# Optimization experiments

Hardware: AMD Instinct MI355X
Metric: run time of the kernel (lower is better)

Reference implementation:

```python
import jax, jax.numpy as jnp
import numpy as np

EPS = 1e-5  # torch GroupNorm default
KNN_K = 16


def _knn_idx(Q, P, K):
    # Q:[B,Nq,3], P:[B,Np,3] -> idx [B,Nq,K], ascending squared distance
    d = (jnp.sum(Q * Q, -1)[:, :, None] + jnp.sum(P * P, -1)[:, None, :]
         - 2.0 * jnp.einsum('bqc,bkc->bqk', Q, P))
    _, idx = jax.lax.top_k(-d, K)
    return idx


def _gather_nbr(feat_bnc, idx_bqk):
    # feat:[B,Np,C], idx:[B,Nq,K] -> [B,Nq,K,C]  (knn_gather)
    return jax.vmap(lambda f, i: f[i])(feat_bnc, idx_bqk)


def _group_norm(x_bcnk, gamma, beta, num_groups=8):
    B, C, N, K = x_bcnk.shape
    G = min(num_groups, C)
    xg = x_bcnk.reshape(B, G, C // G, N, K)
    mu = xg.mean(axis=(2, 3, 4), keepdims=True)
    var = xg.var(axis=(2, 3, 4), keepdims=True)
    xn = ((xg - mu) / jnp.sqrt(var + EPS)).reshape(B, C, N, K)
    return xn * gamma[None, :, None, None] + beta[None, :, None, None]


def _edge_conv(Fq_bcn, Fk_bcn, Pq_b3n, Pk_b3n, k, W, gamma, beta):
    # EdgeConv: concat(x_j - x_i, x_i) -> conv1x1 -> GN -> ReLU -> max over K
    idx = _knn_idx(Pq_b3n.transpose(0, 2, 1), Pk_b3n.transpose(0, 2, 1), k)
    nbr = _gather_nbr(Fk_bcn.transpose(0, 2, 1), idx)          # [B,Nq,K,Cin]
    Fi = jnp.broadcast_to(Fq_bcn.transpose(0, 2, 1)[:, :, None, :], nbr.shape)
    pair = jnp.concatenate([nbr - Fi, Fi], axis=-1)            # [B,Nq,K,2Cin]
    out = jnp.einsum('oc,bnkc->bonk', W, pair)                 # conv 1x1, no bias
    out = _group_norm(out, gamma, beta)
    out = jax.nn.relu(out)
    return out.max(axis=-1)                                    # [B,Cout,Nq]


def _fps_idx(P_b3n, m):
    # Farthest point sampling starting at index 0 (pytorch3d default)
    def one(Pn3):
        d0 = jnp.sum((Pn3 - Pn3[0]) ** 2, -1)
        def step(dists, _):
            nxt = jnp.argmax(dists)
            d = jnp.sum((Pn3 - Pn3[nxt]) ** 2, -1)
            return jnp.minimum(dists, d), nxt
        _, idxs = jax.lax.scan(step, d0, None, length=m - 1)
        return jnp.concatenate([jnp.zeros((1,), jnp.int32), idxs.astype(jnp.int32)])
    return jax.vmap(one)(P_b3n.transpose(0, 2, 1))


def _gather_bcn(x_bcn, idx_bm):
    return jax.vmap(lambda x, i: x[:, i])(x_bcn, idx_bm)


def setup_inputs() -> dict:
    key = jax.random.key(0)
    ks = jax.random.split(key, 8)
    B, N = 2, 8192
    def w(k, shape, s=0.1):
        return jax.random.normal(k, shape, jnp.float32) * s
    return {
        'xyz': jax.random.normal(ks[0], (B, 3, N), jnp.float32),
        'stem_w': w(ks[1], (8, 3)), 'stem_b': jnp.zeros((8,), jnp.float32),
        'w1': w(ks[2], (32, 16)),  'g1': jnp.ones((32,), jnp.float32),  'b1': jnp.zeros((32,), jnp.float32),
        'w2': w(ks[3], (64, 64)),  'g2': jnp.ones((64,), jnp.float32),  'b2': jnp.zeros((64,), jnp.float32),
        'w3': w(ks[4], (64, 128)), 'g3': jnp.ones((64,), jnp.float32),  'b3': jnp.zeros((64,), jnp.float32),
        'w4': w(ks[5], (128, 128)),'g4': jnp.ones((128,), jnp.float32), 'b4': jnp.zeros((128,), jnp.float32),
    }


def reference(xyz, stem_w, stem_b, w1, g1, b1, w2, g2, b2, w3, g3, b3, w4, g4, b4):
    K = KNN_K
    P0 = xyz                                                     # [B,3,N0]
    F0 = jnp.einsum('oc,bcn->bon', stem_w, xyz) + stem_b[None, :, None]
    F0a = _edge_conv(F0, F0, P0, P0, K, w1, g1, b1)              # [B,32,N0]
    N0 = P0.shape[2]
    N1 = max(1, N0 // 4)
    idx1 = _fps_idx(P0, N1)
    P1 = _gather_bcn(P0, idx1)
    F1sk = _gather_bcn(F0a, idx1)
    F1a = _edge_conv(F1sk, F0a, P1, P0, K, w2, g2, b2)           # [B,64,N1]
    N2 = max(1, N1 // 4)
    idx2 = _fps_idx(P1, N2)
    P2 = _gather_bcn(P1, idx2)
    F2sk = _gather_bcn(F1a, idx2)
    F2mid = _edge_conv(F2sk, F1a, P2, P1, K, w3, g3, b3)         # [B,64,N2]
    F2a = _edge_conv(F2mid, F1a, P2, P1, K, w4, g4, b4)          # [B,128,N2]
    return (P0, F0a, P1, F1a, P2, F2a)
```

## Files before the change

kernel.cpp:

```cpp
#include <hip/hip_runtime.h>
#include <math.h>

typedef unsigned long long ull;

__global__ __launch_bounds__(256) void stem_fused(const float* __restrict__ xyz,
    const float* __restrict__ w, const float* __restrict__ bias,
    float* __restrict__ F0, float* __restrict__ P0o, int N){
  int id = blockIdx.x*256 + threadIdx.x;
  int n = id % N; int b = id / N;
  float x = xyz[((size_t)b*3+0)*N+n];
  float y = xyz[((size_t)b*3+1)*N+n];
  float z = xyz[((size_t)b*3+2)*N+n];
  P0o[((size_t)b*3+0)*N+n] = x;
  P0o[((size_t)b*3+1)*N+n] = y;
  P0o[((size_t)b*3+2)*N+n] = z;
  #pragma unroll
  for (int o=0;o<8;o++){
    float v = fmaf(w[o*3+0],x, fmaf(w[o*3+1],y, fmaf(w[o*3+2],z, bias[o])));
    F0[((size_t)b*8+o)*N+n] = v;
  }
}

__global__ __launch_bounds__(256) void knn_fused(
    const float* __restrict__ Pq, const float* __restrict__ Pp,
    int* __restrict__ idxk, int Nq, int Np){
  __shared__ float4 tile[4][256];
  __shared__ float  pd[16][4][64];
  __shared__ int    pi[16][4][64];
  int t = threadIdx.x, w = t>>6, l = t&63;
  int b = blockIdx.y;
  int qn = blockIdx.x*64 + l;
  const float* Pqb = Pq + (size_t)b*3*Nq;
  const float* Ppb = Pp + (size_t)b*3*Np;
  float qx = Pqb[qn], qy = Pqb[Nq+qn], qz = Pqb[2*Nq+qn];
  float qq = __fadd_rn(__fadd_rn(__fmul_rn(qx,qx),__fmul_rn(qy,qy)),__fmul_rn(qz,qz));

  float dl[16]; int il[16];
  #pragma unroll
  for (int u=0;u<16;u++){ dl[u]=INFINITY; il[u]=-1; }
  float maxd = INFINITY; int maxslot = 0;

  int CANDS = Np >> 2;
  int c0 = w*CANDS;
  for (int tb=0; tb<CANDS; tb+=256){
    __syncthreads();
    #pragma unroll
    for (int k=0;k<4;k++){
      int p = c0 + tb + k*64 + l;
      float px = Ppb[p], py = Ppb[Np+p], pz = Ppb[2*Np+p];
      float pp = __fadd_rn(__fadd_rn(__fmul_rn(px,px),__fmul_rn(py,py)),__fmul_rn(pz,pz));
      tile[w][k*64+l] = make_float4(px,py,pz,pp);
    }
    __syncthreads();
    for (int j=0;j<256;j++){
      float4 c = tile[w][j];
      float dot = __fadd_rn(__fadd_rn(__fmul_rn(qx,c.x),__fmul_rn(qy,c.y)),__fmul_rn(qz,c.z));
      float dc  = __fsub_rn(__fadd_rn(qq,c.w), __fmul_rn(2.0f,dot));
      if (dc < maxd){
        int pidx = c0 + tb + j;
        #pragma unroll
        for (int u=0;u<16;u++){ bool sel=(maxslot==u); dl[u]=sel?dc:dl[u]; il[u]=sel?pidx:il[u]; }
        maxd = dl[0]; maxslot = 0;
        #pragma unroll
        for (int u=1;u<16;u++){ bool g=(dl[u]>maxd); maxd=g?dl[u]:maxd; maxslot=g?u:maxslot; }
      }
    }
  }
  #pragma unroll
  for (int u=0;u<16;u++){ pd[u][w][l]=dl[u]; pi[u][w][l]=il[u]; }
  __syncthreads();
  if (t < 64){
    int q = t;
    float mdl[16]; int mil[16];
    #pragma unroll
    for (int u=0;u<16;u++){ mdl[u]=INFINITY; mil[u]=0x7fffffff; }
    float mmaxd = INFINITY; int mmaxi = 0x7fffffff; int mslot = 0;
    for (int s=0;s<4;s++){
      #pragma unroll
      for (int u=0;u<16;u++){
        float d = pd[u][s][q]; int ii = pi[u][s][q];
        bool better = (d < mmaxd) || (d == mmaxd && ii < mmaxi);
        if (better){
          #pragma unroll
          for (int v=0;v<16;v++){ bool sel=(mslot==v); mdl[v]=sel?d:mdl[v]; mil[v]=sel?ii:mil[v]; }
          mmaxd = mdl[0]; mmaxi = mil[0]; mslot = 0;
          #pragma unroll
          for (int v=1;v<16;v++){
            bool g = (mdl[v]>mmaxd) || (mdl[v]==mmaxd && mil[v]>mmaxi);
            mmaxd=g?mdl[v]:mmaxd; mmaxi=g?mil[v]:mmaxi; mslot=g?v:mslot;
          }
        }
      }
    }
    #pragma unroll
    for (int u=0;u<16;u++)
      idxk[((size_t)b*Nq + blockIdx.x*64 + q)*16 + u] = mil[u];
  }
}

template<int CIN, int COUT>
__global__ __launch_bounds__(1024) void edge_conv_pre(
    const float* __restrict__ Fk, const float* __restrict__ Fi,
    const int* __restrict__ idx, const float* __restrict__ W,
    float* __restrict__ pre, int Nq, int Np){
  constexpr int C2  = 2*CIN;
  constexpr int PAD = C2 + 4;
  constexpr int TO  = (COUT <= 64) ? COUT : 64;
  constexpr int OP  = COUT / TO;
  extern __shared__ float sm[];
  float* Wl = sm;
  float* Pl = sm + COUT*PAD;
  int t = threadIdx.x;
  int n = blockIdx.x, b = blockIdx.y;
  for (int e=t; e<COUT*C2; e += blockDim.x){
    int o=e/C2, c=e%C2; Wl[o*PAD+c] = W[e];
  }
  const int* idxn = idx + ((size_t)b*Nq + n)*16;
  for (int e=t; e<16*C2; e += blockDim.x){
    int k = e/C2, c = e%C2;
    int cc = (c < CIN) ? c : (c-CIN);
    float fi = Fi[((size_t)b*CIN + cc)*Nq + n];
    float v;
    if (c < CIN){ int nb = idxn[k]; v = Fk[((size_t)b*CIN + c)*Np + nb] - fi; }
    else v = fi;
    Pl[k*PAD+c] = v;
  }
  __syncthreads();
  int k = t & 15, o0 = t >> 4;
  #pragma unroll
  for (int op=0; op<OP; op++){
    int o = o0 + op*TO;
    float acc = 0.f;
    #pragma unroll
    for (int c=0;c<C2;c+=4){
      float4 wv = *(const float4*)&Wl[o*PAD+c];
      float4 pv = *(const float4*)&Pl[k*PAD+c];
      acc = fmaf(wv.x,pv.x,acc); acc = fmaf(wv.y,pv.y,acc);
      acc = fmaf(wv.z,pv.z,acc); acc = fmaf(wv.w,pv.w,acc);
    }
    pre[(((size_t)b*COUT + o)*Nq + n)*16 + k] = acc;
  }
}

template<int COUT>
__global__ __launch_bounds__(1024) void gn_fused(const float* __restrict__ pre,
    const float* __restrict__ gamma, const float* __restrict__ beta,
    float* __restrict__ outF, int Nq){
  constexpr int CPG = COUT/8;
  int g = blockIdx.x, b = blockIdx.y, t = threadIdx.x;
  size_t base = (((size_t)b*COUT + g*CPG)*(size_t)Nq)*16;
  const float* p = pre + base;
  int len = CPG*Nq*16;
  double s=0.0, sq=0.0;
  for (int i = t*4; i < len; i += 4096){
    float4 v = *(const float4*)(p+i);
    s += (double)v.x; sq = fma((double)v.x,(double)v.x,sq);
    s += (double)v.y; sq = fma((double)v.y,(double)v.y,sq);
    s += (double)v.z; sq = fma((double)v.z,(double)v.z,sq);
    s += (double)v.w; sq = fma((double)v.w,(double)v.w,sq);
  }
  #pragma unroll
  for (int off=32; off>=1; off>>=1){ s += __shfl_down(s, off); sq += __shfl_down(sq, off); }
  __shared__ double ls[16], lq[16];
  __shared__ float stats[2];
  int wid = t>>6;
  if ((t&63)==0){ ls[wid]=s; lq[wid]=sq; }
  __syncthreads();
  if (t==0){
    double S=0.0, Q=0.0;
    #pragma unroll
    for (int w=0;w<16;w++){ S+=ls[w]; Q+=lq[w]; }
    double cnt = (double)CPG*(double)Nq*16.0;
    double mu  = S/cnt;
    double var = Q/cnt - mu*mu;
    stats[0] = (float)mu;
    stats[1] = (float)(1.0/sqrt(var+1e-5));
  }
  __syncthreads();
  float muf = stats[0], rstd = stats[1];
  int outs = CPG*Nq;
  for (int e=t; e<outs; e+=1024){
    int ol = e/Nq, n = e - ol*Nq;
    int o = g*CPG + ol;
    float ga = gamma[o], be = beta[o];
    const float4* pp = (const float4*)(p + (size_t)e*16);
    float m = 0.f;
    #pragma unroll
    for (int q=0;q<4;q++){
      float4 v = pp[q];
      m = fmaxf(m, fmaf((v.x-muf)*rstd, ga, be));
      m = fmaxf(m, fmaf((v.y-muf)*rstd, ga, be));
      m = fmaxf(m, fmaf((v.z-muf)*rstd, ga, be));
      m = fmaxf(m, fmaf((v.w-muf)*rstd, ga, be));
    }
    outF[((size_t)b*COUT + o)*Nq + n] = m;
  }
}

template<int CTRL>
__device__ __forceinline__ float dpp_maxf(float x){
  int y = __builtin_amdgcn_update_dpp(0, __float_as_int(x), CTRL, 0xf, 0xf, true);
  return fmaxf(x, __int_as_float(y));
}

template<int PPT, int BLK, int M>
__global__ __launch_bounds__(BLK, 1) void fps_kernel(const float* __restrict__ P,
    int* __restrict__ idx_out){
  constexpr int N  = PPT*BLK;
  constexpr int NW = BLK/64;
  extern __shared__ __align__(16) float sm[];
  float* lx = sm; float* ly = sm+N; float* lz = sm+2*N;
  ull* wk = (ull*)(sm + 3*N);
  int b = blockIdx.x, t = threadIdx.x;
  const float* Pb = P + (size_t)b*3*N;
  for (int i=t; i<N; i+=BLK){ lx[i]=Pb[i]; ly[i]=Pb[N+i]; lz[i]=Pb[2*N+i]; }
  __syncthreads();
  float px[PPT], py[PPT], pz[PPT], dist[PPT];
  #pragma unroll
  for (int j=0;j<PPT;j++){ int p=t*PPT+j; px[j]=lx[p]; py[j]=ly[p]; pz[j]=lz[p]; }
  #pragma unroll
  for (int j=0;j<PPT;j++){
    asm volatile("" : "+v"(px[j]), "+v"(py[j]), "+v"(pz[j]));
  }
  float sx = lx[0], sy = ly[0], sz = lz[0];
  float bd = -1.f; int bj = 0;
  #pragma unroll
  for (int j=0;j<PPT;j++){
    float dx=__fsub_rn(px[j],sx), dy=__fsub_rn(py[j],sy), dz=__fsub_rn(pz[j],sz);
    float dd=__fadd_rn(__fadd_rn(__fmul_rn(dx,dx),__fmul_rn(dy,dy)),__fmul_rn(dz,dz));
    dist[j]=dd;
    bool c = dd > bd; bd = c?dd:bd; bj = c?j:bj;
  }
  int pbest = t*PPT + bj;
  if (t==0) idx_out[(size_t)b*M] = 0;
  int wid = t>>6, lane = t&63, par = 0;
  for (int i=1;i<M;i++){
    float r = bd;
    r = dpp_maxf<0x111>(r); r = dpp_maxf<0x112>(r);
    r = dpp_maxf<0x114>(r); r = dpp_maxf<0x118>(r);
    r = dpp_maxf<0x142>(r); r = dpp_maxf<0x143>(r);
    float wmax = __int_as_float(__builtin_amdgcn_readlane(__float_as_int(r), 63));
    ull msk = __ballot(bd == wmax);
    int srcl = __ffsll(msk) - 1;
    int wp = __builtin_amdgcn_readlane(pbest, srcl);
    if (lane==0)
      wk[par*NW + wid] = ((ull)__float_as_uint(wmax)<<32)
                       | (unsigned)(~(unsigned)wp);
    __syncthreads();
    ull best = wk[par*NW];
    #pragma unroll
    for (int w=1;w<NW;w++){ ull o = wk[par*NW+w]; best = (o>best)?o:best; }
    unsigned widx = ~(unsigned)best;
    if (t==0) idx_out[(size_t)b*M + i] = (int)widx;
    float nsx = lx[widx], nsy = ly[widx], nsz = lz[widx];
    par ^= 1;
    float nbd = -1.f; int nbj = 0;
    #pragma unroll
    for (int j=0;j<PPT;j++){
      float dx=__fsub_rn(px[j],nsx), dy=__fsub_rn(py[j],nsy), dz=__fsub_rn(pz[j],nsz);
      float dd=__fadd_rn(__fadd_rn(__fmul_rn(dx,dx),__fmul_rn(dy,dy)),__fmul_rn(dz,dz));
      float nd = fminf(dist[j], dd);
      dist[j] = nd;
      bool c = nd > nbd; nbd = c?nd:nbd; nbj = c?j:nbj;
    }
    bd = nbd; pbest = t*PPT + nbj;
  }
}

__global__ __launch_bounds__(256) void gather_fused(float* __restrict__ Pdst,
    const float* __restrict__ Psrc, float* __restrict__ Fdst,
    const float* __restrict__ Fsrc, const int* __restrict__ idxv,
    int CF, int Nsrc, int M){
  int per = (3+CF)*M;
  int total = 2*per;
  for (int id = blockIdx.x*256 + threadIdx.x; id < total; id += gridDim.x*256){
    int b = id/per, r = id%per, c = r/M, m = r%M;
    int sn = idxv[(size_t)b*M + m];
    if (c < 3)
      Pdst[((size_t)b*3+c)*M+m] = Psrc[((size_t)b*3+c)*Nsrc+sn];
    else {
      int cf = c-3;
      Fdst[((size_t)b*CF+cf)*M+m] = Fsrc[((size_t)b*CF+cf)*Nsrc+sn];
    }
  }
}

extern "C" void kernel_launch(void* const* d_in, const int* in_sizes, int n_in,
                              void* d_out, int out_size, void* d_ws, size_t ws_size,
                              hipStream_t stream) {
  const float* xyz    = (const float*)d_in[0];
  const float* stem_w = (const float*)d_in[1];
  const float* stem_b = (const float*)d_in[2];
  const float* w1 = (const float*)d_in[3];
  const float* g1 = (const float*)d_in[4];
  const float* b1 = (const float*)d_in[5];
  const float* w2 = (const float*)d_in[6];
  const float* g2 = (const float*)d_in[7];
  const float* b2 = (const float*)d_in[8];
  const float* w3 = (const float*)d_in[9];
  const float* g3 = (const float*)d_in[10];
  const float* b3 = (const float*)d_in[11];
  const float* w4 = (const float*)d_in[12];
  const float* g4 = (const float*)d_in[13];
  const float* b4 = (const float*)d_in[14];

  float* out = (float*)d_out;
  float* P0o  = out + 0;
  float* F0a  = out + 49152;
  float* P1o  = out + 573440;
  float* F1a  = out + 585728;
  float* P2o  = out + 847872;
  float* F2a  = out + 850944;

  char* ws = (char*)d_ws;
  float* F0     = (float*)(ws + 0);
  float* pre    = (float*)(ws + 524288);
  int*   idxk   = (int*)  (ws + 34078720);
  int*   idx1   = (int*)  (ws + 35127296);
  int*   idx2   = (int*)  (ws + 35143680);
  float* F1sk   = (float*)(ws + 35147776);
  float* F2sk   = (float*)(ws + 35672064);
  float* F2mid  = (float*)(ws + 35934208);

  size_t smem_c1 = (size_t)(32*20  + 16*20 )*4;
  size_t smem_c2 = (size_t)(64*68  + 16*68 )*4;
  size_t smem_c3 = (size_t)(64*132 + 16*132)*4;
  size_t smem_c4 = (size_t)(128*132+ 16*132)*4;
  size_t smem_f1 = (size_t)3*8192*4 + 256;
  size_t smem_f2 = (size_t)3*2048*4 + 256;

  stem_fused<<<64, 256, 0, stream>>>(xyz, stem_w, stem_b, F0, P0o, 8192);
  knn_fused<<<dim3(128,2), 256, 0, stream>>>(xyz, xyz, idxk, 8192, 8192);
  edge_conv_pre<8,32><<<dim3(8192,2), 512, smem_c1, stream>>>(F0, F0, idxk, w1, pre, 8192, 8192);
  gn_fused<32><<<dim3(8,2), 1024, 0, stream>>>(pre, g1, b1, F0a, 8192);

  fps_kernel<32,256,2048><<<2, 256, smem_f1, stream>>>(xyz, idx1);
  gather_fused<<<560, 256, 0, stream>>>(P1o, xyz, F1sk, F0a, idx1, 32, 8192, 2048);

  knn_fused<<<dim3(32,2), 256, 0, stream>>>(P1o, xyz, idxk, 2048, 8192);
  edge_conv_pre<32,64><<<dim3(2048,2), 1024, smem_c2, stream>>>(F0a, F1sk, idxk, w2, pre, 2048, 8192);
  gn_fused<64><<<dim3(8,2), 1024, 0, stream>>>(pre, g2, b2, F1a, 2048);

  fps_kernel<8,256,512><<<2, 256, smem_f2, stream>>>(P1o, idx2);
  gather_fused<<<268, 256, 0, stream>>>(P2o, P1o, F2sk, F1a, idx2, 64, 2048, 512);

  knn_fused<<<dim3(8,2), 256, 0, stream>>>(P2o, P1o, idxk, 512, 2048);
  edge_conv_pre<64,64><<<dim3(512,2), 1024, smem_c3, stream>>>(F1a, F2sk, idxk, w3, pre, 512, 2048);
  gn_fused<64><<<dim3(8,2), 1024, 0, stream>>>(pre, g3, b3, F2mid, 512);

  edge_conv_pre<64,128><<<dim3(512,2), 1024, smem_c4, stream>>>(F1a, F2mid, idxk, w4, pre, 512, 2048);
  gn_fused<128><<<dim3(8,2), 1024, 0, stream>>>(pre, g4, b4, F2a, 512);

  (void)in_sizes; (void)n_in; (void)out_size; (void)ws_size;
}
```

Before: 3.484 ms.

## Fuse GroupNorm partial stats into edge conv and split FPS argmax chains

Each edge-conv block now reduces sum and sum-of-squares for its outputs with wave shuffles and writes per-group partials. A small combine kernel turns these into mean and rstd, and a fully parallel apply kernel does normalize, ReLU and max-over-K. This replaces the old 16-block GroupNorm kernel, which reread the whole pre-activation buffer twice with too few blocks. FPS also splits its per-thread argmax into four independent chains to shorten the dependency chain in the serial loop, at the cost of float partial sums and workspace aliasing of the partial buffers.

```diff
diff --git a/kernel.cpp b/kernel.cpp
--- a/kernel.cpp
+++ b/kernel.cpp
@@ -102,11 +102,14 @@
 __global__ __launch_bounds__(1024) void edge_conv_pre(
     const float* __restrict__ Fk, const float* __restrict__ Fi,
     const int* __restrict__ idx, const float* __restrict__ W,
-    float* __restrict__ pre, int Nq, int Np){
+    float* __restrict__ pre, float* __restrict__ partS,
+    float* __restrict__ partQ, int pstride, int Nq, int Np){
   constexpr int C2  = 2*CIN;
   constexpr int PAD = C2 + 4;
   constexpr int TO  = (COUT <= 64) ? COUT : 64;
   constexpr int OP  = COUT / TO;
+  constexpr int CPG = COUT/8;
+  constexpr int WPG = CPG/4;
   extern __shared__ float sm[];
   float* Wl = sm;
   float* Pl = sm + COUT*PAD;
@@ -127,6 +130,7 @@
   }
   __syncthreads();
   int k = t & 15, o0 = t >> 4;
+  float accv[OP];
   #pragma unroll
   for (int op=0; op<OP; op++){
     int o = o0 + op*TO;
@@ -138,63 +142,68 @@
       acc = fmaf(wv.x,pv.x,acc); acc = fmaf(wv.y,pv.y,acc);
       acc = fmaf(wv.z,pv.z,acc); acc = fmaf(wv.w,pv.w,acc);
     }
+    accv[op] = acc;
     pre[(((size_t)b*COUT + o)*Nq + n)*16 + k] = acc;
   }
-}
-
-template<int COUT>
-__global__ __launch_bounds__(1024) void gn_fused(const float* __restrict__ pre,
-    const float* __restrict__ gamma, const float* __restrict__ beta,
-    float* __restrict__ outF, int Nq){
-  constexpr int CPG = COUT/8;
-  int g = blockIdx.x, b = blockIdx.y, t = threadIdx.x;
-  size_t base = (((size_t)b*COUT + g*CPG)*(size_t)Nq)*16;
-  const float* p = pre + base;
-  int len = CPG*Nq*16;
-  double s=0.0, sq=0.0;
-  for (int i = t*4; i < len; i += 4096){
-    float4 v = *(const float4*)(p+i);
-    s += (double)v.x; sq = fma((double)v.x,(double)v.x,sq);
-    s += (double)v.y; sq = fma((double)v.y,(double)v.y,sq);
-    s += (double)v.z; sq = fma((double)v.z,(double)v.z,sq);
-    s += (double)v.w; sq = fma((double)v.w,(double)v.w,sq);
-  }
-  #pragma unroll
-  for (int off=32; off>=1; off>>=1){ s += __shfl_down(s, off); sq += __shfl_down(sq, off); }
-  __shared__ double ls[16], lq[16];
-  __shared__ float stats[2];
+  int w = t>>6;
+  #pragma unroll
+  for (int op=0; op<OP; op++){
+    float s1 = accv[op], s2 = accv[op]*accv[op];
+    #pragma unroll
+    for (int off=32; off>=1; off>>=1){ s1 += __shfl_down(s1,off); s2 += __shfl_down(s2,off); }
+    if ((t&63)==0){
+      int o = o0 + op*TO;
+      int g = o / CPG;
+      int slot = n*WPG + (w % WPG);
+      partS[((size_t)(b*8+g))*pstride + slot] = s1;
+      partQ[((size_t)(b*8+g))*pstride + slot] = s2;
+    }
+  }
+}
+
+__global__ __launch_bounds__(256) void gn_combine(const float* __restrict__ partS,
+    const float* __restrict__ partQ, float2* __restrict__ stats,
+    int nslot, int pstride, double cnt){
+  int bg = blockIdx.x, t = threadIdx.x;
+  const float* ps = partS + (size_t)bg*pstride;
+  const float* pq = partQ + (size_t)bg*pstride;
+  double s=0.0, q=0.0;
+  for (int i=t; i<nslot; i+=256){ s += (double)ps[i]; q += (double)pq[i]; }
+  #pragma unroll
+  for (int off=32; off>=1; off>>=1){ s += __shfl_down(s,off); q += __shfl_down(q,off); }
+  __shared__ double ls[4], lq[4];
   int wid = t>>6;
-  if ((t&63)==0){ ls[wid]=s; lq[wid]=sq; }
+  if ((t&63)==0){ ls[wid]=s; lq[wid]=q; }
   __syncthreads();
   if (t==0){
-    double S=0.0, Q=0.0;
-    #pragma unroll
-    for (int w=0;w<16;w++){ S+=ls[w]; Q+=lq[w]; }
-    double cnt = (double)CPG*(double)Nq*16.0;
-    double mu  = S/cnt;
+    double S=ls[0]+ls[1]+ls[2]+ls[3], Q=lq[0]+lq[1]+lq[2]+lq[3];
+    double mu = S/cnt;
     double var = Q/cnt - mu*mu;
-    stats[0] = (float)mu;
-    stats[1] = (float)(1.0/sqrt(var+1e-5));
-  }
-  __syncthreads();
-  float muf = stats[0], rstd = stats[1];
-  int outs = CPG*Nq;
-  for (int e=t; e<outs; e+=1024){
-    int ol = e/Nq, n = e - ol*Nq;
-    int o = g*CPG + ol;
-    float ga = gamma[o], be = beta[o];
-    const float4* pp = (const float4*)(p + (size_t)e*16);
-    float m = 0.f;
-    #pragma unroll
-    for (int q=0;q<4;q++){
-      float4 v = pp[q];
-      m = fmaxf(m, fmaf((v.x-muf)*rstd, ga, be));
-      m = fmaxf(m, fmaf((v.y-muf)*rstd, ga, be));
-      m = fmaxf(m, fmaf((v.z-muf)*rstd, ga, be));
-      m = fmaxf(m, fmaf((v.w-muf)*rstd, ga, be));
-    }
-    outF[((size_t)b*COUT + o)*Nq + n] = m;
-  }
+    stats[bg] = make_float2((float)mu, (float)(1.0/sqrt(var+1e-5)));
+  }
+}
+
+template<int COUT>
+__global__ __launch_bounds__(256) void gn_apply(const float* __restrict__ pre,
+    const float2* __restrict__ stats, const float* __restrict__ gamma,
+    const float* __restrict__ beta, float* __restrict__ outF, int Nq){
+  int id = blockIdx.x*256 + threadIdx.x;
+  int o = (id/Nq)%COUT; int b = id/(Nq*COUT);
+  int g = o/(COUT/8);
+  float2 st = stats[b*8+g];
+  float muf = st.x, rstd = st.y;
+  float ga=gamma[o], be=beta[o];
+  const float4* p = (const float4*)(pre + (size_t)id*16);
+  float m = 0.f;
+  #pragma unroll
+  for (int q=0;q<4;q++){
+    float4 v = p[q];
+    m = fmaxf(m, fmaf((v.x-muf)*rstd, ga, be));
+    m = fmaxf(m, fmaf((v.y-muf)*rstd, ga, be));
+    m = fmaxf(m, fmaf((v.z-muf)*rstd, ga, be));
+    m = fmaxf(m, fmaf((v.w-muf)*rstd, ga, be));
+  }
+  outF[id] = m;
 }
 
 template<int CTRL>
@@ -208,6 +217,7 @@
     int* __restrict__ idx_out){
   constexpr int N  = PPT*BLK;
   constexpr int NW = BLK/64;
+  constexpr int Q  = PPT/4;
   extern __shared__ __align__(16) float sm[];
   float* lx = sm; float* ly = sm+N; float* lz = sm+2*N;
   ull* wk = (ull*)(sm + 3*N);
@@ -254,16 +264,23 @@
     if (t==0) idx_out[(size_t)b*M + i] = (int)widx;
     float nsx = lx[widx], nsy = ly[widx], nsz = lz[widx];
     par ^= 1;
-    float nbd = -1.f; int nbj = 0;
+    float nb0=-1.f, nb1=-1.f, nb2=-1.f, nb3=-1.f;
+    int   nj0=0,    nj1=0,    nj2=0,    nj3=0;
     #pragma unroll
     for (int j=0;j<PPT;j++){
       float dx=__fsub_rn(px[j],nsx), dy=__fsub_rn(py[j],nsy), dz=__fsub_rn(pz[j],nsz);
       float dd=__fadd_rn(__fadd_rn(__fmul_rn(dx,dx),__fmul_rn(dy,dy)),__fmul_rn(dz,dz));
       float nd = fminf(dist[j], dd);
       dist[j] = nd;
-      bool c = nd > nbd; nbd = c?nd:nbd; nbj = c?j:nbj;
-    }
-    bd = nbd; pbest = t*PPT + nbj;
+      if (j < Q)        { bool c = nd > nb0; nb0 = c?nd:nb0; nj0 = c?j:nj0; }
+      else if (j < 2*Q) { bool c = nd > nb1; nb1 = c?nd:nb1; nj1 = c?j:nj1; }
+      else if (j < 3*Q) { bool c = nd > nb2; nb2 = c?nd:nb2; nj2 = c?j:nj2; }
+      else              { bool c = nd > nb3; nb3 = c?nd:nb3; nj3 = c?j:nj3; }
+    }
+    bool ca = nb1 > nb0; float ta = ca?nb1:nb0; int tja = ca?nj1:nj0;
+    bool cb = nb3 > nb2; float tb = cb?nb3:nb2; int tjb = cb?nj3:nj2;
+    bool cc = tb > ta;   bd = cc?tb:ta;         int nbj = cc?tjb:tja;
+    pbest = t*PPT + nbj;
   }
 }
 
@@ -316,11 +333,16 @@
   float* F0     = (float*)(ws + 0);
   float* pre    = (float*)(ws + 524288);
   int*   idxk   = (int*)  (ws + 34078720);
-  int*   idx1   = (int*)  (ws + 35127296);
-  int*   idx2   = (int*)  (ws + 35143680);
-  float* F1sk   = (float*)(ws + 35147776);
-  float* F2sk   = (float*)(ws + 35672064);
-  float* F2mid  = (float*)(ws + 35934208);
+  float2* stats = (float2*)(ws + 35127296);
+  int*   idx1   = (int*)  (ws + 35127424);
+  int*   idx2   = (int*)  (ws + 35143808);
+  float* F1sk   = (float*)(ws + 35147904);
+  float* F2sk   = (float*)(ws + 35672192);
+  float* F2mid  = (float*)(ws + 35934336);
+  float* pS1 = (float*)(ws + 35147904);
+  float* pQ1 = (float*)(ws + 35672192);
+  float* pS2 = (float*)(ws + 17825792);
+  float* pQ2 = (float*)(ws + 18087936);
 
   size_t smem_c1 = (size_t)(32*20  + 16*20 )*4;
   size_t smem_c2 = (size_t)(64*68  + 16*68 )*4;
@@ -331,25 +353,29 @@
 
   stem_fused<<<64, 256, 0, stream>>>(xyz, stem_w, stem_b, F0, P0o, 8192);
   knn_fused<<<dim3(128,2), 256, 0, stream>>>(xyz, xyz, idxk, 8192, 8192);
-  edge_conv_pre<8,32><<<dim3(8192,2), 512, smem_c1, stream>>>(F0, F0, idxk, w1, pre, 8192, 8192);
-  gn_fused<32><<<dim3(8,2), 1024, 0, stream>>>(pre, g1, b1, F0a, 8192);
+  edge_conv_pre<8,32><<<dim3(8192,2), 512, smem_c1, stream>>>(F0, F0, idxk, w1, pre, pS1, pQ1, 8192, 8192, 8192);
+  gn_combine<<<16, 256, 0, stream>>>(pS1, pQ1, stats, 8192, 8192, 524288.0);
+  gn_apply<32><<<2048, 256, 0, stream>>>(pre, stats, g1, b1, F0a, 8192);
 
   fps_kernel<32,256,2048><<<2, 256, smem_f1, stream>>>(xyz, idx1);
   gather_fused<<<560, 256, 0, stream>>>(P1o, xyz, F1sk, F0a, idx1, 32, 8192, 2048);
 
   knn_fused<<<dim3(32,2), 256, 0, stream>>>(P1o, xyz, idxk, 2048, 8192);
-  edge_conv_pre<32,64><<<dim3(2048,2), 1024, smem_c2, stream>>>(F0a, F1sk, idxk, w2, pre, 2048, 8192);
-  gn_fused<64><<<dim3(8,2), 1024, 0, stream>>>(pre, g2, b2, F1a, 2048);
+  edge_conv_pre<32,64><<<dim3(2048,2), 1024, smem_c2, stream>>>(F0a, F1sk, idxk, w2, pre, pS2, pQ2, 4096, 2048, 8192);
+  gn_combine<<<16, 256, 0, stream>>>(pS2, pQ2, stats, 4096, 4096, 262144.0);
+  gn_apply<64><<<1024, 256, 0, stream>>>(pre, stats, g2, b2, F1a, 2048);
 
   fps_kernel<8,256,512><<<2, 256, smem_f2, stream>>>(P1o, idx2);
   gather_fused<<<268, 256, 0, stream>>>(P2o, P1o, F2sk, F1a, idx2, 64, 2048, 512);
 
   knn_fused<<<dim3(8,2), 256, 0, stream>>>(P2o, P1o, idxk, 512, 2048);
-  edge_conv_pre<64,64><<<dim3(512,2), 1024, smem_c3, stream>>>(F1a, F2sk, idxk, w3, pre, 512, 2048);
-  gn_fused<64><<<dim3(8,2), 1024, 0, stream>>>(pre, g3, b3, F2mid, 512);
-
-  edge_conv_pre<64,128><<<dim3(512,2), 1024, smem_c4, stream>>>(F1a, F2mid, idxk, w4, pre, 512, 2048);
-  gn_fused<128><<<dim3(8,2), 1024, 0, stream>>>(pre, g4, b4, F2a, 512);
+  edge_conv_pre<64,64><<<dim3(512,2), 1024, smem_c3, stream>>>(F1a, F2sk, idxk, w3, pre, pS2, pQ2, 4096, 512, 2048);
+  gn_combine<<<16, 256, 0, stream>>>(pS2, pQ2, stats, 1024, 4096, 65536.0);
+  gn_apply<64><<<256, 256, 0, stream>>>(pre, stats, g3, b3, F2mid, 512);
+
+  edge_conv_pre<64,128><<<dim3(512,2), 1024, smem_c4, stream>>>(F1a, F2mid, idxk, w4, pre, pS2, pQ2, 4096, 512, 2048);
+  gn_combine<<<16, 256, 0, stream>>>(pS2, pQ2, stats, 2048, 4096, 131072.0);
+  gn_apply<128><<<512, 256, 0, stream>>>(pre, stats, g4, b4, F2a, 512);
 
   (void)in_sizes; (void)n_in; (void)out_size; (void)ws_size;
 }
```

Measured after the change: 3.490 ms. Within noise of the previous version (+0.2%).
